# Kernel tuning notes

Hardware: AMD Instinct MI355X
Metric: run time of the kernel (lower is better)

Reference implementation:

```python
import jax, jax.numpy as jnp
import numpy as np

LATENT = 128
N_NODES = 50000
N_EDGES = 800000
LN_EPS = 1e-5


def _glorot(key, fan_in, fan_out):
    lim = np.sqrt(6.0 / (fan_in + fan_out)).astype(np.float32)
    return jax.random.uniform(key, (fan_in, fan_out), jnp.float32, -lim, lim)


def setup_inputs() -> dict:
    key = jax.random.key(0)
    ks = jax.random.split(key, 10)
    node_latents = jax.random.normal(ks[0], (1, N_NODES, LATENT), jnp.float32)
    mesh_edge_latents = jax.random.normal(ks[1], (1, N_EDGES, LATENT), jnp.float32)
    senders = jax.random.randint(ks[2], (N_EDGES,), 0, N_NODES, jnp.int32)
    receivers = jax.random.randint(ks[3], (N_EDGES,), 0, N_NODES, jnp.int32)
    # mesh_edge_net: Linear(3L, L), ReLU, Linear(L, L), ReLU, LayerNorm(L)
    me_w1 = _glorot(ks[4], 3 * LATENT, LATENT)
    me_b1 = jnp.zeros((LATENT,), jnp.float32)
    me_w2 = _glorot(ks[5], LATENT, LATENT)
    me_b2 = jnp.zeros((LATENT,), jnp.float32)
    me_g = jnp.ones((LATENT,), jnp.float32)
    me_beta = jnp.zeros((LATENT,), jnp.float32)
    # node_feature_net: Linear(2L, L), ReLU, Linear(L, L), ReLU, LayerNorm(L)
    nf_w1 = _glorot(ks[6], 2 * LATENT, LATENT)
    nf_b1 = jnp.zeros((LATENT,), jnp.float32)
    nf_w2 = _glorot(ks[7], LATENT, LATENT)
    nf_b2 = jnp.zeros((LATENT,), jnp.float32)
    nf_g = jnp.ones((LATENT,), jnp.float32)
    nf_beta = jnp.zeros((LATENT,), jnp.float32)
    return dict(node_latents=node_latents, mesh_edge_latents=mesh_edge_latents,
                senders=senders, receivers=receivers,
                me_w1=me_w1, me_b1=me_b1, me_w2=me_w2, me_b2=me_b2, me_g=me_g, me_beta=me_beta,
                nf_w1=nf_w1, nf_b1=nf_b1, nf_w2=nf_w2, nf_b2=nf_b2, nf_g=nf_g, nf_beta=nf_beta)


def _mlp_ln(x, w1, b1, w2, b2, g, beta):
    h = jax.nn.relu(x @ w1 + b1)
    h = jax.nn.relu(h @ w2 + b2)
    mu = jnp.mean(h, axis=-1, keepdims=True)
    var = jnp.var(h, axis=-1, keepdims=True)
    return (h - mu) * jax.lax.rsqrt(var + LN_EPS) * g + beta


def reference(node_latents, mesh_edge_latents, senders, receivers,
              me_w1, me_b1, me_w2, me_b2, me_g, me_beta,
              nf_w1, nf_b1, nf_w2, nf_b2, nf_g, nf_beta):
    # gather sender/receiver node features: [B, E, L]
    edge_in = jnp.concatenate([node_latents[:, senders, :],
                               node_latents[:, receivers, :],
                               mesh_edge_latents], axis=-1)
    new_edges = _mlp_ln(edge_in, me_w1, me_b1, me_w2, me_b2, me_g, me_beta)
    # scatter_add messages to receiver nodes along dim=1
    aggr = jax.vmap(lambda e: jax.ops.segment_sum(e, receivers, num_segments=N_NODES))(new_edges)
    node_in = jnp.concatenate([node_latents, aggr], axis=-1)
    new_nodes = _mlp_ln(node_in, nf_w1, nf_b1, nf_w2, nf_b2, nf_g, nf_beta)
    new_nodes = new_nodes + node_latents  # residual
    new_edges = new_edges + mesh_edge_latents  # residual
    return new_nodes, new_edges
```

## Files before the change

kernel.cpp:

```cpp
#include <hip/hip_runtime.h>
#include <stdint.h>

typedef unsigned short u16;
typedef __bf16 bf16x8 __attribute__((ext_vector_type(8)));
typedef float f32x4 __attribute__((ext_vector_type(4)));

#define N_NODES 50000
#define N_EDGES 800000
#define NTILES  (N_EDGES / 64)
#define LN_EPS 1e-5f

__device__ __forceinline__ uint4 pack8(const float* __restrict__ p) {
    const float4 f0 = ((const float4*)p)[0];
    const float4 f1 = ((const float4*)p)[1];
    union { __bf16 b[8]; uint4 q; } t;
    t.b[0] = (__bf16)f0.x; t.b[1] = (__bf16)f0.y; t.b[2] = (__bf16)f0.z; t.b[3] = (__bf16)f0.w;
    t.b[4] = (__bf16)f1.x; t.b[5] = (__bf16)f1.y; t.b[6] = (__bf16)f1.z; t.b[7] = (__bf16)f1.w;
    return t.q;
}

__global__ void pack_weights(const float* __restrict__ w1e, const float* __restrict__ w2e,
                             const float* __restrict__ w1n, const float* __restrict__ w2n,
                             uint4* __restrict__ out)
{
    const int t = blockIdx.x * 256 + threadIdx.x;
    const float* W; int idx;
    if (t < 6144)       { W = w1e; idx = t; }
    else if (t < 8192)  { W = w2e; idx = t - 6144; }
    else if (t < 12288) { W = w1n; idx = t - 8192; }
    else                { W = w2n; idx = t - 12288; }
    const int lane = idx & 63;
    const int col16 = (idx >> 6) & 7;
    const int kb = idx >> 9;
    const int row0 = kb * 32 + (lane >> 4) * 8;
    const int col = col16 * 16 + (lane & 15);
    union { __bf16 b[8]; uint4 q; } v;
#pragma unroll
    for (int j = 0; j < 8; ++j) v.b[j] = (__bf16)W[(size_t)(row0 + j) * 128 + col];
    out[t] = v.q;
}

__global__ void convert_node(const float* __restrict__ node, uint4* __restrict__ node_bf) {
    const int idx = blockIdx.x * 256 + threadIdx.x;
    node_bf[idx] = pack8(node + (size_t)(idx >> 4) * 128 + (idx & 15) * 8);
}

__global__ void hist_kernel(const int* __restrict__ receivers, int* __restrict__ cnt) {
    const int e = blockIdx.x * 256 + threadIdx.x;
    if (e < N_EDGES) atomicAdd(&cnt[receivers[e]], 1);
}

#define SCAN_NB 196
__global__ void scan1(const int* __restrict__ cnt, int* __restrict__ bsum) {
    __shared__ int wsum[4];
    const int i = blockIdx.x * 256 + threadIdx.x;
    int v = (i < N_NODES) ? cnt[i] : 0;
#pragma unroll
    for (int off = 1; off < 64; off <<= 1) v += __shfl_xor(v, off, 64);
    if ((threadIdx.x & 63) == 0) wsum[threadIdx.x >> 6] = v;
    __syncthreads();
    if (threadIdx.x == 0) bsum[blockIdx.x] = wsum[0] + wsum[1] + wsum[2] + wsum[3];
}
__global__ void scan2(const int* __restrict__ bsum, int* __restrict__ boff) {
    __shared__ int s[256];
    const int t = threadIdx.x;
    const int v = (t < SCAN_NB) ? bsum[t] : 0;
    s[t] = v; __syncthreads();
    for (int off = 1; off < 256; off <<= 1) {
        const int u = (t >= off) ? s[t - off] : 0;
        __syncthreads(); s[t] += u; __syncthreads();
    }
    if (t < SCAN_NB) boff[t] = s[t] - v;
}
__global__ void scan3(const int* __restrict__ cnt, const int* __restrict__ boff,
                      int* __restrict__ cursor) {
    __shared__ int s[256];
    const int i = blockIdx.x * 256 + threadIdx.x;
    const int t = threadIdx.x;
    const int v = (i < N_NODES) ? cnt[i] : 0;
    s[t] = v; __syncthreads();
    for (int off = 1; off < 256; off <<= 1) {
        const int u = (t >= off) ? s[t - off] : 0;
        __syncthreads(); s[t] += u; __syncthreads();
    }
    if (i < N_NODES) cursor[i] = boff[blockIdx.x] + s[t] - v;
}

__global__ void scatter_kernel(const int* __restrict__ senders, const int* __restrict__ receivers,
                               int* __restrict__ cursor,
                               int* __restrict__ sorted_eid, int* __restrict__ pos_of,
                               int* __restrict__ snd_sorted, int* __restrict__ rcv_sorted) {
    const int e = blockIdx.x * 256 + threadIdx.x;
    if (e < N_EDGES) {
        const int rc = receivers[e];
        const int pos = atomicAdd(&cursor[rc], 1);
        sorted_eid[pos] = e;
        pos_of[e] = pos;
        snd_sorted[pos] = senders[e];
        rcv_sorted[pos] = rc;
    }
}

__global__ void permute_elat(const float* __restrict__ elat, const int* __restrict__ pos_of,
                             uint4* __restrict__ elat_s) {
    const int idx = blockIdx.x * 256 + threadIdx.x;
    const int e = idx >> 4, ch = idx & 15;
    const int p = pos_of[e];
    elat_s[(size_t)p * 16 + ch] = pack8(elat + (size_t)e * 128 + ch * 8);
}

template<int SORTED>
__global__ __launch_bounds__(256, 3)
void edge_mlp_kernel(const u16* __restrict__ node_bf, const float* __restrict__ elat,
                     const u16* __restrict__ elat_s,
                     const int* __restrict__ senders, const int* __restrict__ receivers,
                     const int* __restrict__ sorted_eid,
                     const int* __restrict__ snd_sorted, const int* __restrict__ rcv_sorted,
                     const float* __restrict__ b1, const float* __restrict__ b2,
                     const float* __restrict__ gam, const float* __restrict__ bet,
                     const uint4* __restrict__ w1p, const uint4* __restrict__ w2p,
                     float* __restrict__ eout, float* __restrict__ aggr)
{
    __shared__ __align__(16) u16 x_lds[3 * 64 * 128];
    __shared__ int rcv_s[64];
    __shared__ int eid_s[64];
    __shared__ float2 part[256];
    __shared__ float muv[64], rsv[64];

    float* lnf = (float*)x_lds;

    const int tid = threadIdx.x;
    const int w = tid >> 6;
    const int lane = tid & 63;
    const int cl = lane & 15;
    const int q = lane >> 4;
    const int n_base = w * 32;

    float b1v[2], b2v[2], gv[2], bv[2];
#pragma unroll
    for (int n = 0; n < 2; ++n) {
        const int c = n_base + n * 16 + cl;
        b1v[n] = b1[c]; b2v[n] = b2[c];
        gv[n]  = gam[c]; bv[n] = bet[c];
    }

    const int nchunk = gridDim.x;
    const int chunk = (blockIdx.x & 7) * (nchunk >> 3) + (blockIdx.x >> 3);
    const int t_lo = (int)(((long long)chunk * NTILES) / nchunk);
    const int t_hi = (int)(((long long)(chunk + 1) * NTILES) / nchunk);

    for (int tile = t_lo; tile < t_hi; ++tile) {
        const int base = tile * 64;

        {
            const int ch = tid & 15;
            const int r0 = tid >> 4;
#pragma unroll
            for (int gp = 0; gp < 4; ++gp) {
                const int row = gp * 16 + r0;
                const int rx = row & 7;
                const int p = base + row;
                int sn, rc, eid;
                if (SORTED) {
                    sn = snd_sorted[p]; rc = rcv_sorted[p]; eid = sorted_eid[p];
                } else {
                    sn = senders[p]; rc = receivers[p]; eid = p;
                }
                if (ch == 0) { rcv_s[row] = rc; eid_s[row] = eid; }
                uint4* dst = (uint4*)x_lds + row * 16;
                dst[ch ^ rx]          = ((const uint4*)(node_bf + (size_t)sn * 128))[ch];
                dst[1024 + (ch ^ rx)] = ((const uint4*)(node_bf + (size_t)rc * 128))[ch];
                if (SORTED)
                    dst[2048 + (ch ^ rx)] = ((const uint4*)(elat_s + (size_t)p * 128))[ch];
                else
                    dst[2048 + (ch ^ rx)] = pack8(elat + (size_t)p * 128 + ch * 8);
            }
        }
        __syncthreads();

        f32x4 acc[4][2];
#pragma unroll
        for (int m = 0; m < 4; ++m)
#pragma unroll
            for (int n = 0; n < 2; ++n)
#pragma unroll
                for (int r = 0; r < 4; ++r) acc[m][n][r] = 0.f;

        uint4 wreg[14][2];
#pragma unroll
        for (int kb = 0; kb < 2; ++kb)
#pragma unroll
            for (int n = 0; n < 2; ++n)
                wreg[kb][n] = w1p[(kb * 8 + w * 2 + n) * 64 + lane];

#pragma unroll
        for (int kb = 0; kb < 12; ++kb) {
            if (kb + 2 < 12) {
#pragma unroll
                for (int n = 0; n < 2; ++n)
                    wreg[kb + 2][n] = w1p[((kb + 2) * 8 + w * 2 + n) * 64 + lane];
            }
            const int p = kb >> 2, k2 = kb & 3;
            bf16x8 a[4];
#pragma unroll
            for (int m = 0; m < 4; ++m) {
                const int row = m * 16 + cl;
                a[m] = __builtin_bit_cast(bf16x8,
                    ((const uint4*)x_lds)[p * 1024 + row * 16 + ((k2 * 4 + q) ^ (row & 7))]);
            }
#pragma unroll
            for (int m = 0; m < 4; ++m)
#pragma unroll
                for (int n = 0; n < 2; ++n)
                    acc[m][n] = __builtin_amdgcn_mfma_f32_16x16x32_bf16(
                        a[m], __builtin_bit_cast(bf16x8, wreg[kb][n]), acc[m][n], 0, 0, 0);
        }

        uint4 w2reg[4][2];
#pragma unroll
        for (int kb = 0; kb < 4; ++kb)
#pragma unroll
            for (int n = 0; n < 2; ++n)
                w2reg[kb][n] = w2p[(kb * 8 + w * 2 + n) * 64 + lane];

        __syncthreads();

        {
            __bf16* hb = (__bf16*)x_lds;
#pragma unroll
            for (int m = 0; m < 4; ++m)
#pragma unroll
                for (int n = 0; n < 2; ++n)
#pragma unroll
                    for (int r = 0; r < 4; ++r) {
                        const int row = m * 16 + q * 4 + r;
                        const int col = n_base + n * 16 + cl;
                        hb[row * 128 + (((col >> 3) ^ (row & 7)) << 3) + (col & 7)] =
                            (__bf16)fmaxf(acc[m][n][r] + b1v[n], 0.f);
                    }
        }
        __syncthreads();

#pragma unroll
        for (int m = 0; m < 4; ++m)
#pragma unroll
            for (int n = 0; n < 2; ++n)
#pragma unroll
                for (int r = 0; r < 4; ++r) acc[m][n][r] = 0.f;
#pragma unroll
        for (int kb = 0; kb < 4; ++kb) {
            bf16x8 a[4];
#pragma unroll
            for (int m = 0; m < 4; ++m) {
                const int row = m * 16 + cl;
                a[m] = __builtin_bit_cast(bf16x8,
                    ((const uint4*)x_lds)[row * 16 + ((kb * 4 + q) ^ (row & 7))]);
            }
#pragma unroll
            for (int m = 0; m < 4; ++m)
#pragma unroll
                for (int n = 0; n < 2; ++n)
                    acc[m][n] = __builtin_amdgcn_mfma_f32_16x16x32_bf16(
                        a[m], __builtin_bit_cast(bf16x8, w2reg[kb][n]), acc[m][n], 0, 0, 0);
        }

#pragma unroll
        for (int m = 0; m < 4; ++m)
#pragma unroll
            for (int n = 0; n < 2; ++n)
#pragma unroll
                for (int r = 0; r < 4; ++r)
                    acc[m][n][r] = fmaxf(acc[m][n][r] + b2v[n], 0.f);

#pragma unroll
        for (int m = 0; m < 4; ++m)
#pragma unroll
            for (int r = 0; r < 4; ++r) {
                float s  = acc[m][0][r] + acc[m][1][r];
                float ss = acc[m][0][r] * acc[m][0][r] + acc[m][1][r] * acc[m][1][r];
#pragma unroll
                for (int off = 1; off < 16; off <<= 1) {
                    s  += __shfl_xor(s, off, 64);
                    ss += __shfl_xor(ss, off, 64);
                }
                if (cl == 0) part[w * 64 + m * 16 + q * 4 + r] = make_float2(s, ss);
            }
        __syncthreads();
        if (tid < 64) {
            float s = 0.f, ss = 0.f;
#pragma unroll
            for (int ww = 0; ww < 4; ++ww) { const float2 pp = part[ww * 64 + tid]; s += pp.x; ss += pp.y; }
            const float mu = s * (1.f / 128.f);
            const float var = ss * (1.f / 128.f) - mu * mu;
            muv[tid] = mu;
            rsv[tid] = rsqrtf(var + LN_EPS);
        }
        __syncthreads();

#pragma unroll
        for (int m = 0; m < 4; ++m)
#pragma unroll
            for (int r = 0; r < 4; ++r) {
                const int row = m * 16 + q * 4 + r;
                const float mu = muv[row];
                const float rs = rsv[row];
                float* orow = eout + (size_t)eid_s[row] * 128;
#pragma unroll
                for (int n = 0; n < 2; ++n) {
                    const int col = n_base + n * 16 + cl;
                    const float ln = (acc[m][n][r] - mu) * rs * gv[n] + bv[n];
                    lnf[row * 128 + col] = ln;
                    const float e = (float)((__bf16*)x_lds)[16384 + row * 128 + (((col >> 3) ^ (row & 7)) << 3) + (col & 7)];
                    orow[col] = ln + e;
                }
            }
        __syncthreads();

        {
            const int c = tid & 127;
            const int h = tid >> 7;
            const int rstart = h * 32, rend = rstart + 32;
            float sacc = 0.f; int flushed = 0;
#pragma unroll 1
            for (int r = rstart; r < rend; ++r) {
                sacc += lnf[r * 128 + c];
                const int rc = rcv_s[r];
                const bool last = (r == 63);
                const bool bnd = last || (rc != rcv_s[r + 1]);
                if (bnd) {
                    float* dst = &aggr[(size_t)rc * 128 + c];
                    if (SORTED && !last && flushed) *dst = sacc;
                    else atomicAdd(dst, sacc);
                    sacc = 0.f; flushed = 1;
                }
            }
            if (sacc != 0.f)
                atomicAdd(&aggr[(size_t)rcv_s[rend - 1] * 128 + c], sacc);
        }
        __syncthreads();
    }
}

__global__ __launch_bounds__(256, 4)
void node_mlp_kernel(const float* __restrict__ node, const float* __restrict__ aggr,
                     const float* __restrict__ b1, const float* __restrict__ b2,
                     const float* __restrict__ gam, const float* __restrict__ bet,
                     const uint4* __restrict__ w1p, const uint4* __restrict__ w2p,
                     float* __restrict__ nout)
{
    __shared__ __align__(16) u16 x_lds[2 * 64 * 128];
    __shared__ float2 part[256];
    __shared__ float muv[64], rsv[64];

    const int tid = threadIdx.x;
    const int w = tid >> 6;
    const int lane = tid & 63;
    const int cl = lane & 15;
    const int q = lane >> 4;
    const int n_base = w * 32;

    float b1v[2], b2v[2], gv[2], bv[2];
#pragma unroll
    for (int n = 0; n < 2; ++n) {
        const int c = n_base + n * 16 + cl;
        b1v[n] = b1[c]; b2v[n] = b2[c];
        gv[n]  = gam[c]; bv[n] = bet[c];
    }

    const int ntiles = (N_NODES + 63) / 64;
    for (int tile = blockIdx.x; tile < ntiles; tile += gridDim.x) {
        const int base = tile * 64;

        {
            const int ch = tid & 15;
            const int r0 = tid >> 4;
#pragma unroll
            for (int gp = 0; gp < 4; ++gp) {
                const int row = gp * 16 + r0;
                const int rx = row & 7;
                int gn = base + row;
                if (gn >= N_NODES) gn = N_NODES - 1;
                uint4* dst = (uint4*)x_lds + row * 16;
                dst[ch ^ rx]          = pack8(node + (size_t)gn * 128 + ch * 8);
                dst[1024 + (ch ^ rx)] = pack8(aggr + (size_t)gn * 128 + ch * 8);
            }
        }
        __syncthreads();

        f32x4 acc[4][2];
#pragma unroll
        for (int m = 0; m < 4; ++m)
#pragma unroll
            for (int n = 0; n < 2; ++n)
#pragma unroll
                for (int r = 0; r < 4; ++r) acc[m][n][r] = 0.f;

        uint4 wreg[10][2];
#pragma unroll
        for (int kb = 0; kb < 2; ++kb)
#pragma unroll
            for (int n = 0; n < 2; ++n)
                wreg[kb][n] = w1p[(kb * 8 + w * 2 + n) * 64 + lane];

#pragma unroll
        for (int kb = 0; kb < 8; ++kb) {
            if (kb + 2 < 8) {
#pragma unroll
                for (int n = 0; n < 2; ++n)
                    wreg[kb + 2][n] = w1p[((kb + 2) * 8 + w * 2 + n) * 64 + lane];
            }
            const int p = kb >> 2, k2 = kb & 3;
            bf16x8 a[4];
#pragma unroll
            for (int m = 0; m < 4; ++m) {
                const int row = m * 16 + cl;
                a[m] = __builtin_bit_cast(bf16x8,
                    ((const uint4*)x_lds)[p * 1024 + row * 16 + ((k2 * 4 + q) ^ (row & 7))]);
            }
#pragma unroll
            for (int m = 0; m < 4; ++m)
#pragma unroll
                for (int n = 0; n < 2; ++n)
                    acc[m][n] = __builtin_amdgcn_mfma_f32_16x16x32_bf16(
                        a[m], __builtin_bit_cast(bf16x8, wreg[kb][n]), acc[m][n], 0, 0, 0);
        }

        uint4 w2reg[4][2];
#pragma unroll
        for (int kb = 0; kb < 4; ++kb)
#pragma unroll
            for (int n = 0; n < 2; ++n)
                w2reg[kb][n] = w2p[(kb * 8 + w * 2 + n) * 64 + lane];

        __syncthreads();

        {
            __bf16* hb = (__bf16*)(x_lds + 8192);
#pragma unroll
            for (int m = 0; m < 4; ++m)
#pragma unroll
                for (int n = 0; n < 2; ++n)
#pragma unroll
                    for (int r = 0; r < 4; ++r) {
                        const int row = m * 16 + q * 4 + r;
                        const int col = n_base + n * 16 + cl;
                        hb[row * 128 + (((col >> 3) ^ (row & 7)) << 3) + (col & 7)] =
                            (__bf16)fmaxf(acc[m][n][r] + b1v[n], 0.f);
                    }
        }
        __syncthreads();

#pragma unroll
        for (int m = 0; m < 4; ++m)
#pragma unroll
            for (int n = 0; n < 2; ++n)
#pragma unroll
                for (int r = 0; r < 4; ++r) acc[m][n][r] = 0.f;
#pragma unroll
        for (int kb = 0; kb < 4; ++kb) {
            bf16x8 a[4];
#pragma unroll
            for (int m = 0; m < 4; ++m) {
                const int row = m * 16 + cl;
                a[m] = __builtin_bit_cast(bf16x8,
                    ((const uint4*)x_lds)[1024 + row * 16 + ((kb * 4 + q) ^ (row & 7))]);
            }
#pragma unroll
            for (int m = 0; m < 4; ++m)
#pragma unroll
                for (int n = 0; n < 2; ++n)
                    acc[m][n] = __builtin_amdgcn_mfma_f32_16x16x32_bf16(
                        a[m], __builtin_bit_cast(bf16x8, w2reg[kb][n]), acc[m][n], 0, 0, 0);
        }
#pragma unroll
        for (int m = 0; m < 4; ++m)
#pragma unroll
            for (int n = 0; n < 2; ++n)
#pragma unroll
                for (int r = 0; r < 4; ++r)
                    acc[m][n][r] = fmaxf(acc[m][n][r] + b2v[n], 0.f);

#pragma unroll
        for (int m = 0; m < 4; ++m)
#pragma unroll
            for (int r = 0; r < 4; ++r) {
                float s  = acc[m][0][r] + acc[m][1][r];
                float ss = acc[m][0][r] * acc[m][0][r] + acc[m][1][r] * acc[m][1][r];
#pragma unroll
                for (int off = 1; off < 16; off <<= 1) {
                    s  += __shfl_xor(s, off, 64);
                    ss += __shfl_xor(ss, off, 64);
                }
                if (cl == 0) part[w * 64 + m * 16 + q * 4 + r] = make_float2(s, ss);
            }
        __syncthreads();
        if (tid < 64) {
            float s = 0.f, ss = 0.f;
#pragma unroll
            for (int ww = 0; ww < 4; ++ww) { const float2 pp = part[ww * 64 + tid]; s += pp.x; ss += pp.y; }
            const float mu = s * (1.f / 128.f);
            const float var = ss * (1.f / 128.f) - mu * mu;
            muv[tid] = mu;
            rsv[tid] = rsqrtf(var + LN_EPS);
        }
        __syncthreads();

#pragma unroll
        for (int m = 0; m < 4; ++m)
#pragma unroll
            for (int r = 0; r < 4; ++r) {
                const int row = m * 16 + q * 4 + r;
                if (base + row < N_NODES) {
                    const float mu = muv[row];
                    const float rs = rsv[row];
                    float* orow = nout + (size_t)(base + row) * 128;
#pragma unroll
                    for (int n = 0; n < 2; ++n) {
                        const int col = n_base + n * 16 + cl;
                        const float ln = (acc[m][n][r] - mu) * rs * gv[n] + bv[n];
                        const float e = (float)((__bf16*)x_lds)[row * 128 + (((col >> 3) ^ (row & 7)) << 3) + (col & 7)];
                        orow[col] = ln + e;
                    }
                }
            }
        __syncthreads();
    }
}

extern "C" void kernel_launch(void* const* d_in, const int* in_sizes, int n_in,
                              void* d_out, int out_size, void* d_ws, size_t ws_size,
                              hipStream_t stream) {
    (void)in_sizes; (void)n_in; (void)out_size;
    const float* node = (const float*)d_in[0];
    const float* elat = (const float*)d_in[1];
    const int* senders = (const int*)d_in[2];
    const int* receivers = (const int*)d_in[3];
    const float* me_w1 = (const float*)d_in[4];
    const float* me_b1 = (const float*)d_in[5];
    const float* me_w2 = (const float*)d_in[6];
    const float* me_b2 = (const float*)d_in[7];
    const float* me_g  = (const float*)d_in[8];
    const float* me_be = (const float*)d_in[9];
    const float* nf_w1 = (const float*)d_in[10];
    const float* nf_b1 = (const float*)d_in[11];
    const float* nf_w2 = (const float*)d_in[12];
    const float* nf_b2 = (const float*)d_in[13];
    const float* nf_g  = (const float*)d_in[14];
    const float* nf_be = (const float*)d_in[15];

    float* out_nodes = (float*)d_out;
    float* out_edges = out_nodes + (size_t)N_NODES * 128;

    char* ob = (char*)d_out;
    u16* node_bf    = (u16*)ob;
    int* sorted_eid = (int*)(ob + 12800000);
    int* pos_of     = (int*)(ob + 16000000);
    int* snd_sorted = (int*)(ob + 19200000);
    int* rcv_sorted = (int*)(ob + 22400000);

    char* ws = (char*)d_ws;
    const size_t off_aggr   = 0;
    const size_t off_wpack  = off_aggr  + (size_t)N_NODES * 128 * sizeof(float);
    const size_t off_cnt    = off_wpack + 14336 * sizeof(uint4);
    const size_t off_cursor = off_cnt   + (size_t)N_NODES * sizeof(int);
    const size_t off_scan   = off_cursor+ (size_t)N_NODES * sizeof(int);
    const size_t off_elat_s = off_scan  + 4096;
    const size_t need_b     = off_cnt;
    const size_t need_a     = off_elat_s + (size_t)N_EDGES * 128 * sizeof(u16);
    if (ws_size < need_b) return;

    float* aggr   = (float*)(ws + off_aggr);
    uint4* wpack  = (uint4*)(ws + off_wpack);
    int*   cnt    = (int*)(ws + off_cnt);
    int*   cursor = (int*)(ws + off_cursor);
    int*   bsum   = (int*)(ws + off_scan);
    int*   boff   = (int*)(ws + off_scan + 2048);
    u16*   elat_s = (u16*)(ws + off_elat_s);
    const bool tier_a = (ws_size >= need_a);

    hipMemsetAsync(aggr, 0, (size_t)N_NODES * 128 * sizeof(float), stream);
    pack_weights<<<56, 256, 0, stream>>>(me_w1, me_w2, nf_w1, nf_w2, wpack);
    convert_node<<<3125, 256, 0, stream>>>(node, (uint4*)node_bf);

    if (tier_a) {
        hipMemsetAsync(cnt, 0, (size_t)N_NODES * sizeof(int), stream);
        hist_kernel<<<(N_EDGES + 255) / 256, 256, 0, stream>>>(receivers, cnt);
        scan1<<<SCAN_NB, 256, 0, stream>>>(cnt, bsum);
        scan2<<<1, 256, 0, stream>>>(bsum, boff);
        scan3<<<SCAN_NB, 256, 0, stream>>>(cnt, boff, cursor);
        scatter_kernel<<<(N_EDGES + 255) / 256, 256, 0, stream>>>(
            senders, receivers, cursor, sorted_eid, pos_of, snd_sorted, rcv_sorted);
        permute_elat<<<50000, 256, 0, stream>>>(elat, pos_of, (uint4*)elat_s);
        edge_mlp_kernel<1><<<768, 256, 0, stream>>>(node_bf, elat, elat_s,
                                                    senders, receivers,
                                                    sorted_eid, snd_sorted, rcv_sorted,
                                                    me_b1, me_b2, me_g, me_be,
                                                    wpack, wpack + 6144,
                                                    out_edges, aggr);
    } else {
        edge_mlp_kernel<0><<<768, 256, 0, stream>>>(node_bf, elat, elat_s,
                                                    senders, receivers,
                                                    sorted_eid, snd_sorted, rcv_sorted,
                                                    me_b1, me_b2, me_g, me_be,
                                                    wpack, wpack + 6144,
                                                    out_edges, aggr);
    }
    node_mlp_kernel<<<782, 256, 0, stream>>>(node, aggr,
                                             nf_b1, nf_b2, nf_g, nf_be,
                                             wpack + 8192, wpack + 12288,
                                             out_nodes);
}
```

Measured before the change: 1.117 ms.

## Precompute per-node sender/receiver projections of first edge layer

Splits the first edge-MLP matmul by linearity: the sender and receiver blocks of W1 are applied once per node in a new proj_nodes kernel, producing bf16 HS/HR tables. The edge kernel then gathers these projected rows, adds them with the bias in fp32 LDS, and runs only the 128-wide edge-latent block of W1. This cuts first-layer MFMA work per edge from K=384 to K=128, and all weights are now held in registers. The cost is a fresh bf16 rounding of the projections, extra workspace, and a larger fp32 LDS buffer. The unsorted fallback path is removed, so the kernel now requires the larger workspace.

```diff
diff --git a/kernel.cpp b/kernel.cpp
--- a/kernel.cpp
+++ b/kernel.cpp
@@ -8,8 +8,15 @@
 #define N_NODES 50000
 #define N_EDGES 800000
 #define NTILES  (N_EDGES / 64)
-#define LN_EPS 1e-5f
-
+#define LN_EPS  1e-5f
+
+__device__ __forceinline__ u16 f2bfu(float f) {
+    __bf16 b = (__bf16)f;
+    return __builtin_bit_cast(u16, b);
+}
+__device__ __forceinline__ float bfu2f(u16 u) {
+    return (float)__builtin_bit_cast(__bf16, u);
+}
 __device__ __forceinline__ uint4 pack8(const float* __restrict__ p) {
     const float4 f0 = ((const float4*)p)[0];
     const float4 f1 = ((const float4*)p)[1];
@@ -42,14 +49,13 @@
 
 __global__ void convert_node(const float* __restrict__ node, uint4* __restrict__ node_bf) {
     const int idx = blockIdx.x * 256 + threadIdx.x;
-    node_bf[idx] = pack8(node + (size_t)(idx >> 4) * 128 + (idx & 15) * 8);
+    node_bf[idx] = pack8(node + (size_t)idx * 8);
 }
 
 __global__ void hist_kernel(const int* __restrict__ receivers, int* __restrict__ cnt) {
     const int e = blockIdx.x * 256 + threadIdx.x;
     if (e < N_EDGES) atomicAdd(&cnt[receivers[e]], 1);
 }
-
 #define SCAN_NB 196
 __global__ void scan1(const int* __restrict__ cnt, int* __restrict__ bsum) {
     __shared__ int wsum[4];
@@ -85,7 +91,6 @@
     }
     if (i < N_NODES) cursor[i] = boff[blockIdx.x] + s[t] - v;
 }
-
 __global__ void scatter_kernel(const int* __restrict__ senders, const int* __restrict__ receivers,
                                int* __restrict__ cursor,
                                int* __restrict__ sorted_eid, int* __restrict__ pos_of,
@@ -100,7 +105,6 @@
         rcv_sorted[pos] = rc;
     }
 }
-
 __global__ void permute_elat(const float* __restrict__ elat, const int* __restrict__ pos_of,
                              uint4* __restrict__ elat_s) {
     const int idx = blockIdx.x * 256 + threadIdx.x;
@@ -109,39 +113,114 @@
     elat_s[(size_t)p * 16 + ch] = pack8(elat + (size_t)e * 128 + ch * 8);
 }
 
-template<int SORTED>
+__global__ void proj_nodes(const u16* __restrict__ node_bf, const uint4* __restrict__ w1p,
+                           uint4* __restrict__ HS, uint4* __restrict__ HR)
+{
+    __shared__ __align__(16) u16 x[64 * 128];
+    __shared__ __align__(16) u16 hout[2 * 64 * 128];
+    const int tid = threadIdx.x;
+    const int w = tid >> 6, lane = tid & 63, cl = lane & 15, q = lane >> 4;
+    const int n_base = w * 32;
+    const int base = blockIdx.x * 64;
+    const int ch = tid & 15;
+#pragma unroll
+    for (int k = 0; k < 4; ++k) {
+        const int item = tid + k * 256, row = item >> 4;
+        int gn = base + row; if (gn >= N_NODES) gn = N_NODES - 1;
+        ((uint4*)x)[row * 16 + (ch ^ (row & 7))] = ((const uint4*)node_bf)[(size_t)gn * 16 + ch];
+    }
+    uint4 wfS[4][2], wfR[4][2];
+#pragma unroll
+    for (int kb = 0; kb < 4; ++kb)
+#pragma unroll
+        for (int n = 0; n < 2; ++n) {
+            wfS[kb][n] = w1p[(kb * 8 + w * 2 + n) * 64 + lane];
+            wfR[kb][n] = w1p[((kb + 4) * 8 + w * 2 + n) * 64 + lane];
+        }
+    __syncthreads();
+    f32x4 aS[4][2], aR[4][2];
+#pragma unroll
+    for (int m = 0; m < 4; ++m)
+#pragma unroll
+        for (int n = 0; n < 2; ++n)
+#pragma unroll
+            for (int r = 0; r < 4; ++r) { aS[m][n][r] = 0.f; aR[m][n][r] = 0.f; }
+#pragma unroll
+    for (int kb = 0; kb < 4; ++kb) {
+        bf16x8 a[4];
+#pragma unroll
+        for (int m = 0; m < 4; ++m) {
+            const int row = m * 16 + cl;
+            a[m] = __builtin_bit_cast(bf16x8, ((const uint4*)x)[row * 16 + ((kb * 4 + q) ^ (row & 7))]);
+        }
+#pragma unroll
+        for (int m = 0; m < 4; ++m)
+#pragma unroll
+            for (int n = 0; n < 2; ++n) {
+                aS[m][n] = __builtin_amdgcn_mfma_f32_16x16x32_bf16(a[m], __builtin_bit_cast(bf16x8, wfS[kb][n]), aS[m][n], 0, 0, 0);
+                aR[m][n] = __builtin_amdgcn_mfma_f32_16x16x32_bf16(a[m], __builtin_bit_cast(bf16x8, wfR[kb][n]), aR[m][n], 0, 0, 0);
+            }
+    }
+#pragma unroll
+    for (int m = 0; m < 4; ++m)
+#pragma unroll
+        for (int n = 0; n < 2; ++n)
+#pragma unroll
+            for (int r = 0; r < 4; ++r) {
+                const int row = m * 16 + q * 4 + r;
+                const int col = n_base + n * 16 + cl;
+                hout[row * 128 + col]        = f2bfu(aS[m][n][r]);
+                hout[8192 + row * 128 + col] = f2bfu(aR[m][n][r]);
+            }
+    __syncthreads();
+#pragma unroll
+    for (int k = 0; k < 4; ++k) {
+        const int item = tid + k * 256, row = item >> 4;
+        const int gn = base + row;
+        if (gn < N_NODES) {
+            HS[(size_t)gn * 16 + ch] = ((const uint4*)hout)[row * 16 + ch];
+            HR[(size_t)gn * 16 + ch] = ((const uint4*)hout)[1024 + row * 16 + ch];
+        }
+    }
+}
+
 __global__ __launch_bounds__(256, 3)
-void edge_mlp_kernel(const u16* __restrict__ node_bf, const float* __restrict__ elat,
-                     const u16* __restrict__ elat_s,
-                     const int* __restrict__ senders, const int* __restrict__ receivers,
-                     const int* __restrict__ sorted_eid,
-                     const int* __restrict__ snd_sorted, const int* __restrict__ rcv_sorted,
-                     const float* __restrict__ b1, const float* __restrict__ b2,
-                     const float* __restrict__ gam, const float* __restrict__ bet,
-                     const uint4* __restrict__ w1p, const uint4* __restrict__ w2p,
-                     float* __restrict__ eout, float* __restrict__ aggr)
+void edge_sum(const u16* __restrict__ HS, const u16* __restrict__ HR,
+              const u16* __restrict__ elat_s,
+              const int* __restrict__ snd_sorted, const int* __restrict__ rcv_sorted,
+              const int* __restrict__ sorted_eid,
+              const float* __restrict__ b1, const float* __restrict__ b2,
+              const float* __restrict__ gam, const float* __restrict__ bet,
+              const uint4* __restrict__ w1p, const uint4* __restrict__ w2p,
+              float* __restrict__ eout, float* __restrict__ aggr)
 {
-    __shared__ __align__(16) u16 x_lds[3 * 64 * 128];
-    __shared__ int rcv_s[64];
-    __shared__ int eid_s[64];
+    __shared__ __align__(16) u16 x_lds[64 * 128];
+    __shared__ float lnf[64 * 132];
+    __shared__ int rcv_s[64], eid_s[64];
     __shared__ float2 part[256];
     __shared__ float muv[64], rsv[64];
 
-    float* lnf = (float*)x_lds;
-
     const int tid = threadIdx.x;
-    const int w = tid >> 6;
-    const int lane = tid & 63;
-    const int cl = lane & 15;
-    const int q = lane >> 4;
+    const int w = tid >> 6, lane = tid & 63, cl = lane & 15, q = lane >> 4;
     const int n_base = w * 32;
-
-    float b1v[2], b2v[2], gv[2], bv[2];
+    const int ch = tid & 15;
+
+    float b1r[8];
+#pragma unroll
+    for (int j = 0; j < 8; ++j) b1r[j] = b1[ch * 8 + j];
+    uint4 w1c[4][2], w2r[4][2];
+#pragma unroll
+    for (int kb = 0; kb < 4; ++kb)
+#pragma unroll
+        for (int n = 0; n < 2; ++n) {
+            w1c[kb][n] = w1p[((kb + 8) * 8 + w * 2 + n) * 64 + lane];
+            w2r[kb][n] = w2p[(kb * 8 + w * 2 + n) * 64 + lane];
+        }
+    float b2v[2], gv[2], bv[2];
 #pragma unroll
     for (int n = 0; n < 2; ++n) {
         const int c = n_base + n * 16 + cl;
-        b1v[n] = b1[c]; b2v[n] = b2[c];
-        gv[n]  = gam[c]; bv[n] = bet[c];
+        b2v[n] = b2[c]; gv[n] = gam[c]; bv[n] = bet[c];
     }
 
     const int nchunk = gridDim.x;
@@ -152,29 +231,20 @@
     for (int tile = t_lo; tile < t_hi; ++tile) {
         const int base = tile * 64;
 
-        {
-            const int ch = tid & 15;
-            const int r0 = tid >> 4;
-#pragma unroll
-            for (int gp = 0; gp < 4; ++gp) {
-                const int row = gp * 16 + r0;
-                const int rx = row & 7;
-                const int p = base + row;
-                int sn, rc, eid;
-                if (SORTED) {
-                    sn = snd_sorted[p]; rc = rcv_sorted[p]; eid = sorted_eid[p];
-                } else {
-                    sn = senders[p]; rc = receivers[p]; eid = p;
-                }
-                if (ch == 0) { rcv_s[row] = rc; eid_s[row] = eid; }
-                uint4* dst = (uint4*)x_lds + row * 16;
-                dst[ch ^ rx]          = ((const uint4*)(node_bf + (size_t)sn * 128))[ch];
-                dst[1024 + (ch ^ rx)] = ((const uint4*)(node_bf + (size_t)rc * 128))[ch];
-                if (SORTED)
-                    dst[2048 + (ch ^ rx)] = ((const uint4*)(elat_s + (size_t)p * 128))[ch];
-                else
-                    dst[2048 + (ch ^ rx)] = pack8(elat + (size_t)p * 128 + ch * 8);
-            }
+#pragma unroll
+        for (int k = 0; k < 4; ++k) {
+            const int item = tid + k * 256, row = item >> 4;
+            const int p = base + row;
+            const int sn = snd_sorted[p];
+            const int rc = rcv_sorted[p];
+            if (ch == 0) { rcv_s[row] = rc; eid_s[row] = sorted_eid[p]; }
+            ((uint4*)x_lds)[row * 16 + (ch ^ (row & 7))] = ((const uint4*)elat_s)[(size_t)p * 16 + ch];
+            union { uint4 q; u16 u[8]; } hs, hr;
+            hs.q = ((const uint4*)HS)[(size_t)sn * 16 + ch];
+            hr.q = ((const uint4*)HR)[(size_t)rc * 16 + ch];
+#pragma unroll
+            for (int j = 0; j < 8; ++j)
+                lnf[row * 132 + ch * 8 + j] = bfu2f(hs.u[j]) + bfu2f(hr.u[j]) + b1r[j];
         }
         __syncthreads();
 
@@ -185,60 +255,54 @@
             for (int n = 0; n < 2; ++n)
 #pragma unroll
                 for (int r = 0; r < 4; ++r) acc[m][n][r] = 0.f;
-
-        uint4 wreg[14][2];
-#pragma unroll
-        for (int kb = 0; kb < 2; ++kb)
-#pragma unroll
-            for (int n = 0; n < 2; ++n)
-                wreg[kb][n] = w1p[(kb * 8 + w * 2 + n) * 64 + lane];
-
-#pragma unroll
-        for (int kb = 0; kb < 12; ++kb) {
-            if (kb + 2 < 12) {
-#pragma unroll
-                for (int n = 0; n < 2; ++n)
-                    wreg[kb + 2][n] = w1p[((kb + 2) * 8 + w * 2 + n) * 64 + lane];
-            }
-            const int p = kb >> 2, k2 = kb & 3;
+#pragma unroll
+        for (int kb = 0; kb < 4; ++kb) {
             bf16x8 a[4];
 #pragma unroll
             for (int m = 0; m < 4; ++m) {
                 const int row = m * 16 + cl;
-                a[m] = __builtin_bit_cast(bf16x8,
-                    ((const uint4*)x_lds)[p * 1024 + row * 16 + ((k2 * 4 + q) ^ (row & 7))]);
+                a[m] = __builtin_bit_cast(bf16x8, ((const uint4*)x_lds)[row * 16 + ((kb * 4 + q) ^ (row & 7))]);
             }
 #pragma unroll
             for (int m = 0; m < 4; ++m)
 #pragma unroll
                 for (int n = 0; n < 2; ++n)
-                    acc[m][n] = __builtin_amdgcn_mfma_f32_16x16x32_bf16(
-                        a[m], __builtin_bit_cast(bf16x8, wreg[kb][n]), acc[m][n], 0, 0, 0);
-        }
-
-        uint4 w2reg[4][2];
-#pragma unroll
-        for (int kb = 0; kb < 4; ++kb)
-#pragma unroll
-            for (int n = 0; n < 2; ++n)
-                w2reg[kb][n] = w2p[(kb * 8 + w * 2 + n) * 64 + lane];
-
-        __syncthreads();
-
-        {
-            __bf16* hb = (__bf16*)x_lds;
-#pragma unroll
-            for (int m = 0; m < 4; ++m)
-#pragma unroll
-                for (int n = 0; n < 2; ++n)
-#pragma unroll
-                    for (int r = 0; r < 4; ++r) {
-                        const int row = m * 16 + q * 4 + r;
-                        const int col = n_base + n * 16 + cl;
-                        hb[row * 128 + (((col >> 3) ^ (row & 7)) << 3) + (col & 7)] =
-                            (__bf16)fmaxf(acc[m][n][r] + b1v[n], 0.f);
-                    }
-        }
+                    acc[m][n] = __builtin_amdgcn_mfma_f32_16x16x32_bf16(a[m], __builtin_bit_cast(bf16x8, w1c[kb][n]), acc[m][n], 0, 0, 0);
+        }
+        unsigned int rp[4][2][2];
+#pragma unroll
+        for (int m = 0; m < 4; ++m)
+#pragma unroll
+            for (int n = 0; n < 2; ++n) {
+#pragma unroll
+                for (int r = 0; r < 4; ++r) {
+                    const int row = m * 16 + q * 4 + r;
+                    const int col = n_base + n * 16 + cl;
+                    acc[m][n][r] = fmaxf(acc[m][n][r] + lnf[row * 132 + col], 0.f);
+                }
+#pragma unroll
+                for (int rr = 0; rr < 2; ++rr) {
+                    const int r0 = rr * 2;
+                    const int row0 = m * 16 + q * 4 + r0;
+                    const int row1 = row0 + 1;
+                    const int col = n_base + n * 16 + cl;
+                    const unsigned int lo = x_lds[row0 * 128 + (((col >> 3) ^ (row0 & 7)) << 3) + (col & 7)];
+                    const unsigned int hi = x_lds[row1 * 128 + (((col >> 3) ^ (row1 & 7)) << 3) + (col & 7)];
+                    rp[m][n][rr] = lo | (hi << 16);
+                }
+            }
+        __syncthreads();
+
+#pragma unroll
+        for (int m = 0; m < 4; ++m)
+#pragma unroll
+            for (int n = 0; n < 2; ++n)
+#pragma unroll
+                for (int r = 0; r < 4; ++r) {
+                    const int row = m * 16 + q * 4 + r;
+                    const int col = n_base + n * 16 + cl;
+                    x_lds[row * 128 + (((col >> 3) ^ (row & 7)) << 3) + (col & 7)] = f2bfu(acc[m][n][r]);
+                }
         __syncthreads();
 
 #pragma unroll
@@ -253,17 +317,14 @@
 #pragma unroll
             for (int m = 0; m < 4; ++m) {
                 const int row = m * 16 + cl;
-                a[m] = __builtin_bit_cast(bf16x8,
-                    ((const uint4*)x_lds)[row * 16 + ((kb * 4 + q) ^ (row & 7))]);
+                a[m] = __builtin_bit_cast(bf16x8, ((const uint4*)x_lds)[row * 16 + ((kb * 4 + q) ^ (row & 7))]);
             }
 #pragma unroll
             for (int m = 0; m < 4; ++m)
 #pragma unroll
                 for (int n = 0; n < 2; ++n)
-                    acc[m][n] = __builtin_amdgcn_mfma_f32_16x16x32_bf16(
-                        a[m], __builtin_bit_cast(bf16x8, w2reg[kb][n]), acc[m][n], 0, 0, 0);
-        }
-
+                    acc[m][n] = __builtin_amdgcn_mfma_f32_16x16x32_bf16(a[m], __builtin_bit_cast(bf16x8, w2r[kb][n]), acc[m][n], 0, 0, 0);
+        }
 #pragma unroll
         for (int m = 0; m < 4; ++m)
 #pragma unroll
@@ -309,9 +370,9 @@
                 for (int n = 0; n < 2; ++n) {
                     const int col = n_base + n * 16 + cl;
                     const float ln = (acc[m][n][r] - mu) * rs * gv[n] + bv[n];
-                    lnf[row * 128 + col] = ln;
-                    const float e = (float)((__bf16*)x_lds)[16384 + row * 128 + (((col >> 3) ^ (row & 7)) << 3) + (col & 7)];
-                    orow[col] = ln + e;
+                    lnf[row * 132 + col] = ln;
+                    const float resv = bfu2f((u16)(rp[m][n][r >> 1] >> ((r & 1) * 16)));
+                    orow[col] = ln + resv;
                 }
             }
         __syncthreads();
@@ -323,13 +384,13 @@
             float sacc = 0.f; int flushed = 0;
 #pragma unroll 1
             for (int r = rstart; r < rend; ++r) {
-                sacc += lnf[r * 128 + c];
+                sacc += lnf[r * 132 + c];
                 const int rc = rcv_s[r];
                 const bool last = (r == 63);
                 const bool bnd = last || (rc != rcv_s[r + 1]);
                 if (bnd) {
                     float* dst = &aggr[(size_t)rc * 128 + c];
-                    if (SORTED && !last && flushed) *dst = sacc;
+                    if (!last && flushed) *dst = sacc;
                     else atomicAdd(dst, sacc);
                     sacc = 0.f; flushed = 1;
                 }
@@ -353,10 +414,7 @@
     __shared__ float muv[64], rsv[64];
 
     const int tid = threadIdx.x;
-    const int w = tid >> 6;
-    const int lane = tid & 63;
-    const int cl = lane & 15;
-    const int q = lane >> 4;
+    const int w = tid >> 6, lane = tid & 63, cl = lane & 15, q = lane >> 4;
     const int n_base = w * 32;
 
     float b1v[2], b2v[2], gv[2], bv[2];
@@ -370,7 +428,6 @@
     const int ntiles = (N_NODES + 63) / 64;
     for (int tile = blockIdx.x; tile < ntiles; tile += gridDim.x) {
         const int base = tile * 64;
-
         {
             const int ch = tid & 15;
             const int r0 = tid >> 4;
@@ -394,14 +451,12 @@
             for (int n = 0; n < 2; ++n)
 #pragma unroll
                 for (int r = 0; r < 4; ++r) acc[m][n][r] = 0.f;
-
         uint4 wreg[10][2];
 #pragma unroll
         for (int kb = 0; kb < 2; ++kb)
 #pragma unroll
             for (int n = 0; n < 2; ++n)
                 wreg[kb][n] = w1p[(kb * 8 + w * 2 + n) * 64 + lane];
-
 #pragma unroll
         for (int kb = 0; kb < 8; ++kb) {
             if (kb + 2 < 8) {
@@ -424,16 +479,13 @@
                     acc[m][n] = __builtin_amdgcn_mfma_f32_16x16x32_bf16(
                         a[m], __builtin_bit_cast(bf16x8, wreg[kb][n]), acc[m][n], 0, 0, 0);
         }
-
         uint4 w2reg[4][2];
 #pragma unroll
         for (int kb = 0; kb < 4; ++kb)
 #pragma unroll
             for (int n = 0; n < 2; ++n)
                 w2reg[kb][n] = w2p[(kb * 8 + w * 2 + n) * 64 + lane];
-
-        __syncthreads();
-
+        __syncthreads();
         {
             __bf16* hb = (__bf16*)(x_lds + 8192);
 #pragma unroll
@@ -449,7 +501,6 @@
                     }
         }
         __syncthreads();
-
 #pragma unroll
         for (int m = 0; m < 4; ++m)
 #pragma unroll
@@ -479,7 +530,6 @@
 #pragma unroll
                 for (int r = 0; r < 4; ++r)
                     acc[m][n][r] = fmaxf(acc[m][n][r] + b2v[n], 0.f);
-
 #pragma unroll
         for (int m = 0; m < 4; ++m)
 #pragma unroll
@@ -504,7 +554,6 @@
             rsv[tid] = rsqrtf(var + LN_EPS);
         }
         __syncthreads();
-
 #pragma unroll
         for (int m = 0; m < 4; ++m)
 #pragma unroll
@@ -560,14 +609,15 @@
 
     char* ws = (char*)d_ws;
     const size_t off_aggr   = 0;
-    const size_t off_wpack  = off_aggr  + (size_t)N_NODES * 128 * sizeof(float);
-    const size_t off_cnt    = off_wpack + 14336 * sizeof(uint4);
-    const size_t off_cursor = off_cnt   + (size_t)N_NODES * sizeof(int);
-    const size_t off_scan   = off_cursor+ (size_t)N_NODES * sizeof(int);
-    const size_t off_elat_s = off_scan  + 4096;
-    const size_t need_b     = off_cnt;
-    const size_t need_a     = off_elat_s + (size_t)N_EDGES * 128 * sizeof(u16);
-    if (ws_size < need_b) return;
+    const size_t off_wpack  = off_aggr   + (size_t)N_NODES * 128 * sizeof(float);
+    const size_t off_cnt    = off_wpack  + 14336 * sizeof(uint4);
+    const size_t off_cursor = off_cnt    + (size_t)N_NODES * sizeof(int);
+    const size_t off_scan   = off_cursor + (size_t)N_NODES * sizeof(int);
+    const size_t off_HS     = off_scan   + 4096;
+    const size_t off_HR     = off_HS     + (size_t)N_NODES * 256;
+    const size_t off_elat_s = off_HR     + (size_t)N_NODES * 256;
+    const size_t need       = off_elat_s + (size_t)N_EDGES * 256;
+    if (ws_size < need) return;
 
     float* aggr   = (float*)(ws + off_aggr);
     uint4* wpack  = (uint4*)(ws + off_wpack);
@@ -575,36 +625,27 @@
     int*   cursor = (int*)(ws + off_cursor);
     int*   bsum   = (int*)(ws + off_scan);
     int*   boff   = (int*)(ws + off_scan + 2048);
+    u16*   HS     = (u16*)(ws + off_HS);
+    u16*   HR     = (u16*)(ws + off_HR);
     u16*   elat_s = (u16*)(ws + off_elat_s);
-    const bool tier_a = (ws_size >= need_a);
 
     hipMemsetAsync(aggr, 0, (size_t)N_NODES * 128 * sizeof(float), stream);
+    hipMemsetAsync(cnt, 0, (size_t)N_NODES * sizeof(int), stream);
     pack_weights<<<56, 256, 0, stream>>>(me_w1, me_w2, nf_w1, nf_w2, wpack);
     convert_node<<<3125, 256, 0, stream>>>(node, (uint4*)node_bf);
-
-    if (tier_a) {
-        hipMemsetAsync(cnt, 0, (size_t)N_NODES * sizeof(int), stream);
-        hist_kernel<<<(N_EDGES + 255) / 256, 256, 0, stream>>>(receivers, cnt);
-        scan1<<<SCAN_NB, 256, 0, stream>>>(cnt, bsum);
-        scan2<<<1, 256, 0, stream>>>(bsum, boff);
-        scan3<<<SCAN_NB, 256, 0, stream>>>(cnt, boff, cursor);
-        scatter_kernel<<<(N_EDGES + 255) / 256, 256, 0, stream>>>(
-            senders, receivers, cursor, sorted_eid, pos_of, snd_sorted, rcv_sorted);
-        permute_elat<<<50000, 256, 0, stream>>>(elat, pos_of, (uint4*)elat_s);
-        edge_mlp_kernel<1><<<768, 256, 0, stream>>>(node_bf, elat, elat_s,
-                                                    senders, receivers,
-                                                    sorted_eid, snd_sorted, rcv_sorted,
-                                                    me_b1, me_b2, me_g, me_be,
-                                                    wpack, wpack + 6144,
-                                                    out_edges, aggr);
-    } else {
-        edge_mlp_kernel<0><<<768, 256, 0, stream>>>(node_bf, elat, elat_s,
-                                                    senders, receivers,
-                                                    sorted_eid, snd_sorted, rcv_sorted,
-                                                    me_b1, me_b2, me_g, me_be,
-                                                    wpack, wpack + 6144,
-                                                    out_edges, aggr);
-    }
+    hist_kernel<<<(N_EDGES + 255) / 256, 256, 0, stream>>>(receivers, cnt);
+    scan1<<<SCAN_NB, 256, 0, stream>>>(cnt, bsum);
+    scan2<<<1, 256, 0, stream>>>(bsum, boff);
+    scan3<<<SCAN_NB, 256, 0, stream>>>(cnt, boff, cursor);
+    scatter_kernel<<<(N_EDGES + 255) / 256, 256, 0, stream>>>(
+        senders, receivers, cursor, sorted_eid, pos_of, snd_sorted, rcv_sorted);
+    proj_nodes<<<(N_NODES + 63) / 64, 256, 0, stream>>>(node_bf, wpack, (uint4*)HS, (uint4*)HR);
+    permute_elat<<<50000, 256, 0, stream>>>(elat, pos_of, (uint4*)elat_s);
+    edge_sum<<<768, 256, 0, stream>>>(HS, HR, elat_s,
+                                      snd_sorted, rcv_sorted, sorted_eid,
+                                      me_b1, me_b2, me_g, me_be,
+                                      wpack, wpack + 6144,
+                                      out_edges, aggr);
     node_mlp_kernel<<<782, 256, 0, stream>>>(node, aggr,
                                              nf_b1, nf_b2, nf_g, nf_be,
                                              wpack + 8192, wpack + 12288,
```

Result: no change. 1.135 ms (+1.6%).
